# Kernel optimization log

Hardware: AMD Instinct MI355X
Metric: run time of the kernel (lower is better)

The kernel has to match this reference:

```python
import jax, jax.numpy as jnp
import numpy as np

NZ = 1024       # opts.nz (== NH so layer-0 input weights stack with other layers)
NH = 1024       # opts.nh
NSTATE = 64     # opts.n_state
NLAYERS = 4
MAX_PRIM_LEN = 100
T = MAX_PRIM_LEN + 1   # max_unroll=True runs exactly max_prim_len+1 steps
P_BIAS = 1.0           # opts.dec_p_bias


def setup_inputs() -> dict:
    key = jax.random.key(0)
    ks = jax.random.split(key, 9)
    s_ih = 1.0 / np.sqrt(NH)
    u = lambda k, shape: jax.random.uniform(k, shape, jnp.float32, -s_ih, s_ih)
    return {
        "z": jax.random.normal(ks[0], (1, NZ), jnp.float32),
        # torch LSTM params, gate order (i, f, g, o); layer0 input dim == NZ == NH
        "Wih": u(ks[1], (NLAYERS, 4 * NH, NH)),
        "Whh": u(ks[2], (NLAYERS, 4 * NH, NH)),
        "bih": u(ks[3], (NLAYERS, 4 * NH)),
        "bhh": u(ks[4], (NLAYERS, 4 * NH)),
        "Ws": u(ks[5], (NSTATE, NH)),
        "bs": u(ks[6], (NSTATE,)),
        "Wp": u(ks[7], (2, NH)),
        "bp": u(ks[8], (2,)),
    }


def reference(z, Wih, Whh, bih, bhh, Ws, bs, Wp, bp):
    z0 = z.reshape(-1)  # (NZ,)
    zeros = jnp.zeros_like(z0)

    def step(carry, i):
        h, c = carry                      # each (NLAYERS, NH)
        x = jnp.where(i == 0, z0, zeros)  # input is z at t=0, zeros after
        hs, cs = [], []
        inp = x
        for l in range(NLAYERS):
            gates = Wih[l] @ inp + bih[l] + Whh[l] @ h[l] + bhh[l]
            gi, gf, gg, go = jnp.split(gates, 4)
            cl = jax.nn.sigmoid(gf) * c[l] + jax.nn.sigmoid(gi) * jnp.tanh(gg)
            hl = jax.nn.sigmoid(go) * jnp.tanh(cl)
            hs.append(hl)
            cs.append(cl)
            inp = hl
        o = inp                            # top-layer output, (NH,)
        s = Ws @ o + bs                    # state head, (NSTATE,)
        logits = (Wp @ o + bp).at[0].add(P_BIAS)
        p = jax.nn.softmax(logits)         # (2,)
        last = i == T - 1                  # torch: t > max_prim_len -> force [0,1]
        p = jnp.where(last, jnp.array([0.0, 1.0], p.dtype), p)
        samp = jnp.where(last, 1, 0).astype(jnp.int64)  # max_unroll forces 0 until last
        return (jnp.stack(hs), jnp.stack(cs)), (s, p, samp)

    h0 = jnp.zeros((NLAYERS, NH), z.dtype)
    _, (states, probs, samples) = jax.lax.scan(step, (h0, h0), jnp.arange(T))
    return states[:, None, :], probs[:, None, :], samples[:, None]
```

## Files before the change

### kernel.cpp

```cpp
#include <hip/hip_runtime.h>


#define TT    101
#define NBLK  256
#define NTH   512
#define NREP  8
#define SLAB_U32 512
#define HB16_BYTES (4 * TT * NREP * SLAB_U32 * 4)
#define OUT_PROBS 6464
#define OUT_SAMP  6666
#define SENT 0xFFFFFFFFu

typedef _Float16 h2 __attribute__((ext_vector_type(2)));

__device__ __forceinline__ h2 mkh2(float a, float b) {
    h2 r; r.x = (_Float16)a; r.y = (_Float16)b; return r;
}
__device__ __forceinline__ unsigned pack2(float a, float b) {
    return __builtin_bit_cast(unsigned, mkh2(a, b));
}
__device__ __forceinline__ h2 as_h2(unsigned u) { return __builtin_bit_cast(h2, u); }

#if __has_builtin(__builtin_amdgcn_fdot2)
__device__ __forceinline__ float fdot2(h2 a, h2 b, float c) {
    return __builtin_amdgcn_fdot2(a, b, c, false);
}
#else
__device__ __forceinline__ float fdot2(h2 a, h2 b, float c) {
    return fmaf((float)a.x, (float)b.x, fmaf((float)a.y, (float)b.y, c));
}
#endif

__device__ __forceinline__ uint4 load16_bypass(const uint4* p) {
    uint4 r;
    asm volatile("global_load_dwordx4 %0, %1, off sc0 sc1\n\ts_waitcnt vmcnt(0)"
                 : "=v"(r) : "v"(p) : "memory");
    return r;
}
__device__ __forceinline__ void store4_bypass(unsigned* p, unsigned v) {
    asm volatile("global_store_dword %0, %1, off sc0 sc1" :: "v"(p), "v"(v) : "memory");
}
__device__ __forceinline__ uint4 poll16(const uint4* p) {
    uint4 r = load16_bypass(p);
    while (r.x == SENT || r.y == SENT || r.z == SENT || r.w == SENT) {
        __builtin_amdgcn_s_sleep(1);
        r = load16_bypass(p);
    }
    return r;
}

__device__ __forceinline__ float wave_sum(float x) {
    int v;
    v = __builtin_amdgcn_update_dpp(0, __builtin_bit_cast(int, x), 0x111, 0xf, 0xf, false);
    x += __builtin_bit_cast(float, v);
    v = __builtin_amdgcn_update_dpp(0, __builtin_bit_cast(int, x), 0x112, 0xf, 0xf, false);
    x += __builtin_bit_cast(float, v);
    v = __builtin_amdgcn_update_dpp(0, __builtin_bit_cast(int, x), 0x114, 0xf, 0xe, false);
    x += __builtin_bit_cast(float, v);
    v = __builtin_amdgcn_update_dpp(0, __builtin_bit_cast(int, x), 0x118, 0xf, 0xc, false);
    x += __builtin_bit_cast(float, v);
    v = __builtin_amdgcn_update_dpp(0, __builtin_bit_cast(int, x), 0x142, 0xa, 0xf, false);
    x += __builtin_bit_cast(float, v);
    v = __builtin_amdgcn_update_dpp(0, __builtin_bit_cast(int, x), 0x143, 0xc, 0xf, false);
    x += __builtin_bit_cast(float, v);
    return __builtin_bit_cast(float, __builtin_amdgcn_readlane(__builtin_bit_cast(int, x), 63));
}

__device__ __forceinline__ float sigm(float x) { return 1.f / (1.f + expf(-x)); }

__global__ __launch_bounds__(NTH, 2) void lstm_kernel(
    const float* __restrict__ z,
    const float* __restrict__ Wih, const float* __restrict__ Whh,
    const float* __restrict__ bih, const float* __restrict__ bhh,
    const float* __restrict__ Ws,  const float* __restrict__ bs,
    const float* __restrict__ Wp,  const float* __restrict__ bp,
    unsigned* __restrict__ hb16, float* __restrict__ out)
{
    const int tid  = threadIdx.x;
    const int wv   = tid >> 6;
    const int lane = tid & 63;
    const int l    = blockIdx.x >> 6;
    const int gb   = blockIdx.x & 63;
    const int uA   = (gb << 4) + (wv << 1);

    __shared__ __align__(16) uint4 vh4[256];
    __shared__ unsigned hout[8];

    h2 w[8][16];
    #pragma unroll
    for (int r = 0; r < 8; ++r) {
        const int u = uA + (r >> 2);
        const int g = r & 3;
        const size_t row = ((size_t)((l << 12) + (g << 10) + u)) << 10;
        const float4* pa = (const float4*)(Whh + row + (lane << 3));
        const float4* pb = (const float4*)(Whh + row + 512 + (lane << 3));
        const float4* pc = (const float4*)(Wih + row + (lane << 3));
        const float4* pd = (const float4*)(Wih + row + 512 + (lane << 3));
        float4 f;
        f = pa[0]; w[r][0]  = mkh2(f.x, f.y); w[r][1]  = mkh2(f.z, f.w);
        f = pa[1]; w[r][2]  = mkh2(f.x, f.y); w[r][3]  = mkh2(f.z, f.w);
        f = pb[0]; w[r][4]  = mkh2(f.x, f.y); w[r][5]  = mkh2(f.z, f.w);
        f = pb[1]; w[r][6]  = mkh2(f.x, f.y); w[r][7]  = mkh2(f.z, f.w);
        f = pc[0]; w[r][8]  = mkh2(f.x, f.y); w[r][9]  = mkh2(f.z, f.w);
        f = pc[1]; w[r][10] = mkh2(f.x, f.y); w[r][11] = mkh2(f.z, f.w);
        f = pd[0]; w[r][12] = mkh2(f.x, f.y); w[r][13] = mkh2(f.z, f.w);
        f = pd[1]; w[r][14] = mkh2(f.x, f.y); w[r][15] = mkh2(f.z, f.w);
    }

    float bA[4], bB[4];
    #pragma unroll
    for (int g = 0; g < 4; ++g) {
        const int iA = (l << 12) + (g << 10) + uA;
        bA[g] = bih[iA] + bhh[iA];
        bB[g] = bih[iA + 1] + bhh[iA + 1];
    }

    const bool role_states = (l == 0 && wv == 6);
    const bool role_probs  = (l == 1 && gb == 0 && wv == 6);
    float hw0[16], hw1[16], hb0 = 0.f, hb1 = 0.f;
    if (role_states) {
        #pragma unroll
        for (int k = 0; k < 16; ++k) hw0[k] = Ws[(gb << 10) + (lane << 4) + k];
        hb0 = bs[gb];
    } else if (role_probs) {
        #pragma unroll
        for (int k = 0; k < 16; ++k) {
            hw0[k] = Wp[(lane << 4) + k];
            hw1[k] = Wp[1024 + (lane << 4) + k];
        }
        hb0 = bp[0]; hb1 = bp[1];
    }
    int th = 0;

    float cstA = 0.f, cstB = 0.f;

    #pragma unroll 1
    for (int t = 0; t < TT; ++t) {
        const bool full = (l > 0) || (t == 0);
        const int rep = (gb + wv) & (NREP - 1);

        if (wv < 2) {
            const int c = (wv << 6) + lane;
            if (t == 0) vh4[c] = make_uint4(0, 0, 0, 0);
            else {
                const uint4* slab = (const uint4*)(hb16 + (size_t)((l * TT + t - 1) * NREP + rep) * SLAB_U32);
                vh4[c] = poll16(slab + c);
            }
        } else if (wv < 4) {
            const int c = ((wv - 2) << 6) + lane;
            if (l > 0) {
                const uint4* slab = (const uint4*)(hb16 + (size_t)(((l - 1) * TT + t) * NREP + rep) * SLAB_U32);
                vh4[128 + c] = poll16(slab + c);
            } else if (t == 0) {
                const float4 f0 = *(const float4*)(z + (c << 3));
                const float4 f1 = *(const float4*)(z + (c << 3) + 4);
                vh4[128 + c] = make_uint4(pack2(f0.x, f0.y), pack2(f0.z, f0.w),
                                          pack2(f1.x, f1.y), pack2(f1.z, f1.w));
            }
        }
        __syncthreads();

        float acc[8] = {0.f, 0.f, 0.f, 0.f, 0.f, 0.f, 0.f, 0.f};
        {
            const uint4 A1 = vh4[lane];
            const uint4 A2 = vh4[64 + lane];
            const unsigned a8[8] = {A1.x, A1.y, A1.z, A1.w, A2.x, A2.y, A2.z, A2.w};
            #pragma unroll
            for (int k = 0; k < 8; ++k) {
                const h2 v2 = as_h2(a8[k]);
                #pragma unroll
                for (int r = 0; r < 8; ++r) acc[r] = fdot2(w[r][k], v2, acc[r]);
            }
            if (full) {
                const uint4 B1 = vh4[128 + lane];
                const uint4 B2 = vh4[192 + lane];
                const unsigned b8[8] = {B1.x, B1.y, B1.z, B1.w, B2.x, B2.y, B2.z, B2.w};
                #pragma unroll
                for (int k = 0; k < 8; ++k) {
                    const h2 v2 = as_h2(b8[k]);
                    #pragma unroll
                    for (int r = 0; r < 8; ++r) acc[r] = fdot2(w[r][8 + k], v2, acc[r]);
                }
            }
        }

        float tot[8];
        #pragma unroll
        for (int r = 0; r < 8; ++r) tot[r] = wave_sum(acc[r]);

        cstA = fmaf(sigm(tot[1] + bA[1]), cstA, sigm(tot[0] + bA[0]) * tanhf(tot[2] + bA[2]));
        cstB = fmaf(sigm(tot[5] + bB[1]), cstB, sigm(tot[4] + bB[0]) * tanhf(tot[6] + bB[2]));
        const float hA = sigm(tot[3] + bA[3]) * tanhf(cstA);
        const float hB = sigm(tot[7] + bB[3]) * tanhf(cstB);
        if (lane == 0) hout[wv] = pack2(hA, hB);
        __syncthreads();

        if (wv == 7) {
            const unsigned val = hout[lane & 7];
            unsigned* addr = hb16 + (size_t)(l * TT + t) * NREP * SLAB_U32
                           + (size_t)(lane >> 3) * SLAB_U32 + (gb << 3) + (lane & 7);
            store4_bypass(addr, val);
        } else if ((role_states || role_probs) && th < TT && th <= t - 3) {
            const int hrep = (gb + th) & (NREP - 1);
            const uint4* slab3 = (const uint4*)(hb16 + (size_t)((3 * TT + th) * NREP + hrep) * SLAB_U32);
            const uint4 r0 = load16_bypass(slab3 + (lane << 1));
            const uint4 r1 = load16_bypass(slab3 + (lane << 1) + 1);
            const bool ok = !(r0.x == SENT || r0.y == SENT || r0.z == SENT || r0.w == SENT ||
                              r1.x == SENT || r1.y == SENT || r1.z == SENT || r1.w == SENT);
            if (__ballot(ok) == ~0ull) {
                const unsigned u8[8] = {r0.x, r0.y, r0.z, r0.w, r1.x, r1.y, r1.z, r1.w};
                if (role_states) {
                    float a = 0.f;
                    #pragma unroll
                    for (int j = 0; j < 8; ++j) {
                        const h2 p = as_h2(u8[j]);
                        a = fmaf(hw0[2 * j], (float)p.x, a);
                        a = fmaf(hw0[2 * j + 1], (float)p.y, a);
                    }
                    const float tots = wave_sum(a);
                    if (lane == 0) out[th * 64 + gb] = tots + hb0;
                } else {
                    float a0 = 0.f, a1 = 0.f;
                    #pragma unroll
                    for (int j = 0; j < 8; ++j) {
                        const h2 p = as_h2(u8[j]);
                        a0 = fmaf(hw0[2 * j], (float)p.x, a0); a0 = fmaf(hw0[2 * j + 1], (float)p.y, a0);
                        a1 = fmaf(hw1[2 * j], (float)p.x, a1); a1 = fmaf(hw1[2 * j + 1], (float)p.y, a1);
                    }
                    const float t0 = wave_sum(a0), t1 = wave_sum(a1);
                    if (lane == 0) {
                        float p0, p1;
                        if (th == TT - 1) { p0 = 0.f; p1 = 1.f; }
                        else {
                            const float l0 = t0 + hb0 + 1.0f;
                            const float l1 = t1 + hb1;
                            const float m  = fmaxf(l0, l1);
                            const float e0 = expf(l0 - m), e1 = expf(l1 - m);
                            const float inv = 1.f / (e0 + e1);
                            p0 = e0 * inv; p1 = e1 * inv;
                        }
                        out[OUT_PROBS + 2 * th]     = p0;
                        out[OUT_PROBS + 2 * th + 1] = p1;
                        out[OUT_SAMP + th] = (th == TT - 1) ? 1.0f : 0.0f;
                    }
                }
                ++th;
            }
        }
    }

    if (role_states || role_probs) {
        while (th < TT) {
            const int hrep = (gb + th) & (NREP - 1);
            const uint4* slab3 = (const uint4*)(hb16 + (size_t)((3 * TT + th) * NREP + hrep) * SLAB_U32);
            const uint4 r0 = poll16(slab3 + (lane << 1));
            const uint4 r1 = poll16(slab3 + (lane << 1) + 1);
            const unsigned u8[8] = {r0.x, r0.y, r0.z, r0.w, r1.x, r1.y, r1.z, r1.w};
            if (role_states) {
                float a = 0.f;
                #pragma unroll
                for (int j = 0; j < 8; ++j) {
                    const h2 p = as_h2(u8[j]);
                    a = fmaf(hw0[2 * j], (float)p.x, a);
                    a = fmaf(hw0[2 * j + 1], (float)p.y, a);
                }
                const float tots = wave_sum(a);
                if (lane == 0) out[th * 64 + gb] = tots + hb0;
            } else {
                float a0 = 0.f, a1 = 0.f;
                #pragma unroll
                for (int j = 0; j < 8; ++j) {
                    const h2 p = as_h2(u8[j]);
                    a0 = fmaf(hw0[2 * j], (float)p.x, a0); a0 = fmaf(hw0[2 * j + 1], (float)p.y, a0);
                    a1 = fmaf(hw1[2 * j], (float)p.x, a1); a1 = fmaf(hw1[2 * j + 1], (float)p.y, a1);
                }
                const float t0 = wave_sum(a0), t1 = wave_sum(a1);
                if (lane == 0) {
                    float p0, p1;
                    if (th == TT - 1) { p0 = 0.f; p1 = 1.f; }
                    else {
                        const float l0 = t0 + hb0 + 1.0f;
                        const float l1 = t1 + hb1;
                        const float m  = fmaxf(l0, l1);
                        const float e0 = expf(l0 - m), e1 = expf(l1 - m);
                        const float inv = 1.f / (e0 + e1);
                        p0 = e0 * inv; p1 = e1 * inv;
                    }
                    out[OUT_PROBS + 2 * th]     = p0;
                    out[OUT_PROBS + 2 * th + 1] = p1;
                    out[OUT_SAMP + th] = (th == TT - 1) ? 1.0f : 0.0f;
                }
            }
            ++th;
        }
    }
}

extern "C" void kernel_launch(void* const* d_in, const int* in_sizes, int n_in,
                              void* d_out, int out_size, void* d_ws, size_t ws_size,
                              hipStream_t stream)
{
    const float* z   = (const float*)d_in[0];
    const float* Wih = (const float*)d_in[1];
    const float* Whh = (const float*)d_in[2];
    const float* bih = (const float*)d_in[3];
    const float* bhh = (const float*)d_in[4];
    const float* Ws  = (const float*)d_in[5];
    const float* bs  = (const float*)d_in[6];
    const float* Wp  = (const float*)d_in[7];
    const float* bp  = (const float*)d_in[8];
    float* out = (float*)d_out;

    unsigned* hb16 = (unsigned*)d_ws;

    hipMemsetAsync(hb16, 0xFF, HB16_BYTES, stream);
    lstm_kernel<<<NBLK, NTH, 0, stream>>>(z, Wih, Whh, bih, bhh,
                                          Ws, bs, Wp, bp, hb16, out);
}
```

Baseline: 512.4 us.

## Move output heads to dedicated blocks, double-buffer LDS, use fast gate math

```diff
diff --git a/kernel.cpp b/kernel.cpp
--- a/kernel.cpp
+++ b/kernel.cpp
@@ -3,10 +3,12 @@
 
 #define TT    101
 #define NBLK  256
+#define NHEAD 65
 #define NTH   512
 #define NREP  8
 #define SLAB_U32 512
-#define HB16_BYTES (4 * TT * NREP * SLAB_U32 * 4)
+#define STEP_U32 (NREP * SLAB_U32)
+#define HB16_BYTES (4 * TT * STEP_U32 * 4)
 #define OUT_PROBS 6464
 #define OUT_SAMP  6666
 #define SENT 0xFFFFFFFFu
@@ -29,6 +31,18 @@
 __device__ __forceinline__ float fdot2(h2 a, h2 b, float c) {
     return fmaf((float)a.x, (float)b.x, fmaf((float)a.y, (float)b.y, c));
 }
+#endif
+
+#if __has_builtin(__builtin_amdgcn_exp2f) && __has_builtin(__builtin_amdgcn_rcpf)
+__device__ __forceinline__ float fsigm(float x) {
+    return __builtin_amdgcn_rcpf(1.f + __builtin_amdgcn_exp2f(-1.442695041f * x));
+}
+__device__ __forceinline__ float ftanh(float x) {
+    return fmaf(-2.f, __builtin_amdgcn_rcpf(1.f + __builtin_amdgcn_exp2f(2.885390082f * x)), 1.f);
+}
+#else
+__device__ __forceinline__ float fsigm(float x) { return 1.f / (1.f + expf(-x)); }
+__device__ __forceinline__ float ftanh(float x) { return tanhf(x); }
 #endif
 
 __device__ __forceinline__ uint4 load16_bypass(const uint4* p) {
@@ -65,8 +79,6 @@
     x += __builtin_bit_cast(float, v);
     return __builtin_bit_cast(float, __builtin_amdgcn_readlane(__builtin_bit_cast(int, x), 63));
 }
-
-__device__ __forceinline__ float sigm(float x) { return 1.f / (1.f + expf(-x)); }
 
 __global__ __launch_bounds__(NTH, 2) void lstm_kernel(
     const float* __restrict__ z,
@@ -79,12 +91,73 @@
     const int tid  = threadIdx.x;
     const int wv   = tid >> 6;
     const int lane = tid & 63;
-    const int l    = blockIdx.x >> 6;
-    const int gb   = blockIdx.x & 63;
-    const int uA   = (gb << 4) + (wv << 1);
-
-    __shared__ __align__(16) uint4 vh4[256];
-    __shared__ unsigned hout[8];
+
+    if (blockIdx.x >= NBLK) {
+        if (wv != 0) return;
+        const int hb  = blockIdx.x - NBLK;
+        const int rep = hb & (NREP - 1);
+        if (hb < 64) {
+            float wr[16];
+            #pragma unroll
+            for (int k = 0; k < 16; ++k) wr[k] = Ws[(hb << 10) + (lane << 4) + k];
+            const float bsv = bs[hb];
+            for (int th = 0; th < TT; ++th) {
+                const uint4* slab = (const uint4*)(hb16 + (size_t)(3 * TT + th) * STEP_U32 + rep * SLAB_U32);
+                const uint4 r0 = poll16(slab + 2 * lane);
+                const uint4 r1 = poll16(slab + 2 * lane + 1);
+                const unsigned u8[8] = {r0.x, r0.y, r0.z, r0.w, r1.x, r1.y, r1.z, r1.w};
+                float a = 0.f;
+                #pragma unroll
+                for (int j = 0; j < 8; ++j) {
+                    const h2 p = as_h2(u8[j]);
+                    a = fmaf(wr[2 * j], (float)p.x, a);
+                    a = fmaf(wr[2 * j + 1], (float)p.y, a);
+                }
+                a = wave_sum(a);
+                if (lane == 0) out[th * 64 + hb] = a + bsv;
+            }
+        } else {
+            for (int i = lane; i < TT; i += 64) out[OUT_SAMP + i] = (i == TT - 1) ? 1.0f : 0.0f;
+            if (lane == 0) { out[OUT_PROBS + 2 * (TT - 1)] = 0.f; out[OUT_PROBS + 2 * (TT - 1) + 1] = 1.f; }
+            float w0[16], w1[16];
+            #pragma unroll
+            for (int k = 0; k < 16; ++k) {
+                w0[k] = Wp[(lane << 4) + k];
+                w1[k] = Wp[1024 + (lane << 4) + k];
+            }
+            const float bp0 = bp[0], bp1 = bp[1];
+            for (int th = 0; th < TT - 1; ++th) {
+                const uint4* slab = (const uint4*)(hb16 + (size_t)(3 * TT + th) * STEP_U32 + rep * SLAB_U32);
+                const uint4 r0 = poll16(slab + 2 * lane);
+                const uint4 r1 = poll16(slab + 2 * lane + 1);
+                const unsigned u8[8] = {r0.x, r0.y, r0.z, r0.w, r1.x, r1.y, r1.z, r1.w};
+                float a0 = 0.f, a1 = 0.f;
+                #pragma unroll
+                for (int j = 0; j < 8; ++j) {
+                    const h2 p = as_h2(u8[j]);
+                    a0 = fmaf(w0[2 * j], (float)p.x, a0); a0 = fmaf(w0[2 * j + 1], (float)p.y, a0);
+                    a1 = fmaf(w1[2 * j], (float)p.x, a1); a1 = fmaf(w1[2 * j + 1], (float)p.y, a1);
+                }
+                a0 = wave_sum(a0); a1 = wave_sum(a1);
+                if (lane == 0) {
+                    const float l0 = a0 + bp0 + 1.0f;
+                    const float l1 = a1 + bp1;
+                    const float m  = fmaxf(l0, l1);
+                    const float e0 = expf(l0 - m), e1 = expf(l1 - m);
+                    const float inv = 1.f / (e0 + e1);
+                    out[OUT_PROBS + 2 * th]     = e0 * inv;
+                    out[OUT_PROBS + 2 * th + 1] = e1 * inv;
+                }
+            }
+        }
+        return;
+    }
+
+    const int l   = blockIdx.x >> 6;
+    const int gb  = blockIdx.x & 63;
+    const int uA  = (gb << 4) + (wv << 1);
+
+    __shared__ __align__(16) uint4 vbuf[2][256];
 
     h2 w[8][16];
     #pragma unroll
@@ -115,43 +188,28 @@
         bB[g] = bih[iA + 1] + bhh[iA + 1];
     }
 
-    const bool role_states = (l == 0 && wv == 6);
-    const bool role_probs  = (l == 1 && gb == 0 && wv == 6);
-    float hw0[16], hw1[16], hb0 = 0.f, hb1 = 0.f;
-    if (role_states) {
-        #pragma unroll
-        for (int k = 0; k < 16; ++k) hw0[k] = Ws[(gb << 10) + (lane << 4) + k];
-        hb0 = bs[gb];
-    } else if (role_probs) {
-        #pragma unroll
-        for (int k = 0; k < 16; ++k) {
-            hw0[k] = Wp[(lane << 4) + k];
-            hw1[k] = Wp[1024 + (lane << 4) + k];
-        }
-        hb0 = bp[0]; hb1 = bp[1];
-    }
-    int th = 0;
-
     float cstA = 0.f, cstB = 0.f;
 
     #pragma unroll 1
     for (int t = 0; t < TT; ++t) {
         const bool full = (l > 0) || (t == 0);
-        const int rep = (gb + wv) & (NREP - 1);
+        uint4* vh4 = vbuf[t & 1];
 
         if (wv < 2) {
             const int c = (wv << 6) + lane;
             if (t == 0) vh4[c] = make_uint4(0, 0, 0, 0);
             else {
-                const uint4* slab = (const uint4*)(hb16 + (size_t)((l * TT + t - 1) * NREP + rep) * SLAB_U32);
+                const int rep = (gb + wv) & (NREP - 1);
+                const uint4* slab = (const uint4*)(hb16 + (size_t)(l * TT + t - 1) * STEP_U32 + rep * SLAB_U32);
                 vh4[c] = poll16(slab + c);
             }
-        } else if (wv < 4) {
+        } else if (wv < 4 && full) {
             const int c = ((wv - 2) << 6) + lane;
             if (l > 0) {
-                const uint4* slab = (const uint4*)(hb16 + (size_t)(((l - 1) * TT + t) * NREP + rep) * SLAB_U32);
+                const int rep = (gb + wv) & (NREP - 1);
+                const uint4* slab = (const uint4*)(hb16 + (size_t)((l - 1) * TT + t) * STEP_U32 + rep * SLAB_U32);
                 vh4[128 + c] = poll16(slab + c);
-            } else if (t == 0) {
+            } else {
                 const float4 f0 = *(const float4*)(z + (c << 3));
                 const float4 f1 = *(const float4*)(z + (c << 3) + 4);
                 vh4[128 + c] = make_uint4(pack2(f0.x, f0.y), pack2(f0.z, f0.w),
@@ -188,110 +246,16 @@
         #pragma unroll
         for (int r = 0; r < 8; ++r) tot[r] = wave_sum(acc[r]);
 
-        cstA = fmaf(sigm(tot[1] + bA[1]), cstA, sigm(tot[0] + bA[0]) * tanhf(tot[2] + bA[2]));
-        cstB = fmaf(sigm(tot[5] + bB[1]), cstB, sigm(tot[4] + bB[0]) * tanhf(tot[6] + bB[2]));
-        const float hA = sigm(tot[3] + bA[3]) * tanhf(cstA);
-        const float hB = sigm(tot[7] + bB[3]) * tanhf(cstB);
-        if (lane == 0) hout[wv] = pack2(hA, hB);
-        __syncthreads();
-
-        if (wv == 7) {
-            const unsigned val = hout[lane & 7];
-            unsigned* addr = hb16 + (size_t)(l * TT + t) * NREP * SLAB_U32
-                           + (size_t)(lane >> 3) * SLAB_U32 + (gb << 3) + (lane & 7);
-            store4_bypass(addr, val);
-        } else if ((role_states || role_probs) && th < TT && th <= t - 3) {
-            const int hrep = (gb + th) & (NREP - 1);
-            const uint4* slab3 = (const uint4*)(hb16 + (size_t)((3 * TT + th) * NREP + hrep) * SLAB_U32);
-            const uint4 r0 = load16_bypass(slab3 + (lane << 1));
-            const uint4 r1 = load16_bypass(slab3 + (lane << 1) + 1);
-            const bool ok = !(r0.x == SENT || r0.y == SENT || r0.z == SENT || r0.w == SENT ||
-                              r1.x == SENT || r1.y == SENT || r1.z == SENT || r1.w == SENT);
-            if (__ballot(ok) == ~0ull) {
-                const unsigned u8[8] = {r0.x, r0.y, r0.z, r0.w, r1.x, r1.y, r1.z, r1.w};
-                if (role_states) {
-                    float a = 0.f;
-                    #pragma unroll
-                    for (int j = 0; j < 8; ++j) {
-                        const h2 p = as_h2(u8[j]);
-                        a = fmaf(hw0[2 * j], (float)p.x, a);
-                        a = fmaf(hw0[2 * j + 1], (float)p.y, a);
-                    }
-                    const float tots = wave_sum(a);
-                    if (lane == 0) out[th * 64 + gb] = tots + hb0;
-                } else {
-                    float a0 = 0.f, a1 = 0.f;
-                    #pragma unroll
-                    for (int j = 0; j < 8; ++j) {
-                        const h2 p = as_h2(u8[j]);
-                        a0 = fmaf(hw0[2 * j], (float)p.x, a0); a0 = fmaf(hw0[2 * j + 1], (float)p.y, a0);
-                        a1 = fmaf(hw1[2 * j], (float)p.x, a1); a1 = fmaf(hw1[2 * j + 1], (float)p.y, a1);
-                    }
-                    const float t0 = wave_sum(a0), t1 = wave_sum(a1);
-                    if (lane == 0) {
-                        float p0, p1;
-                        if (th == TT - 1) { p0 = 0.f; p1 = 1.f; }
-                        else {
-                            const float l0 = t0 + hb0 + 1.0f;
-                            const float l1 = t1 + hb1;
-                            const float m  = fmaxf(l0, l1);
-                            const float e0 = expf(l0 - m), e1 = expf(l1 - m);
-                            const float inv = 1.f / (e0 + e1);
-                            p0 = e0 * inv; p1 = e1 * inv;
-                        }
-                        out[OUT_PROBS + 2 * th]     = p0;
-                        out[OUT_PROBS + 2 * th + 1] = p1;
-                        out[OUT_SAMP + th] = (th == TT - 1) ? 1.0f : 0.0f;
-                    }
-                }
-                ++th;
-            }
-        }
-    }
-
-    if (role_states || role_probs) {
-        while (th < TT) {
-            const int hrep = (gb + th) & (NREP - 1);
-            const uint4* slab3 = (const uint4*)(hb16 + (size_t)((3 * TT + th) * NREP + hrep) * SLAB_U32);
-            const uint4 r0 = poll16(slab3 + (lane << 1));
-            const uint4 r1 = poll16(slab3 + (lane << 1) + 1);
-            const unsigned u8[8] = {r0.x, r0.y, r0.z, r0.w, r1.x, r1.y, r1.z, r1.w};
-            if (role_states) {
-                float a = 0.f;
-                #pragma unroll
-                for (int j = 0; j < 8; ++j) {
-                    const h2 p = as_h2(u8[j]);
-                    a = fmaf(hw0[2 * j], (float)p.x, a);
-                    a = fmaf(hw0[2 * j + 1], (float)p.y, a);
-                }
-                const float tots = wave_sum(a);
-                if (lane == 0) out[th * 64 + gb] = tots + hb0;
-            } else {
-                float a0 = 0.f, a1 = 0.f;
-                #pragma unroll
-                for (int j = 0; j < 8; ++j) {
-                    const h2 p = as_h2(u8[j]);
-                    a0 = fmaf(hw0[2 * j], (float)p.x, a0); a0 = fmaf(hw0[2 * j + 1], (float)p.y, a0);
-                    a1 = fmaf(hw1[2 * j], (float)p.x, a1); a1 = fmaf(hw1[2 * j + 1], (float)p.y, a1);
-                }
-                const float t0 = wave_sum(a0), t1 = wave_sum(a1);
-                if (lane == 0) {
-                    float p0, p1;
-                    if (th == TT - 1) { p0 = 0.f; p1 = 1.f; }
-                    else {
-                        const float l0 = t0 + hb0 + 1.0f;
-                        const float l1 = t1 + hb1;
-                        const float m  = fmaxf(l0, l1);
-                        const float e0 = expf(l0 - m), e1 = expf(l1 - m);
-                        const float inv = 1.f / (e0 + e1);
-                        p0 = e0 * inv; p1 = e1 * inv;
-                    }
-                    out[OUT_PROBS + 2 * th]     = p0;
-                    out[OUT_PROBS + 2 * th + 1] = p1;
-                    out[OUT_SAMP + th] = (th == TT - 1) ? 1.0f : 0.0f;
-                }
-            }
-            ++th;
+        cstA = fmaf(fsigm(tot[1] + bA[1]), cstA, fsigm(tot[0] + bA[0]) * ftanh(tot[2] + bA[2]));
+        cstB = fmaf(fsigm(tot[5] + bB[1]), cstB, fsigm(tot[4] + bB[0]) * ftanh(tot[6] + bB[2]));
+        const float hA = fsigm(tot[3] + bA[3]) * ftanh(cstA);
+        const float hB = fsigm(tot[7] + bB[3]) * ftanh(cstB);
+
+        const unsigned packed = pack2(hA, hB);
+        if (lane < NREP) {
+            unsigned* addr = hb16 + (size_t)(l * TT + t) * STEP_U32
+                           + (lane << 9) + (gb << 3) + wv;
+            store4_bypass(addr, packed);
         }
     }
 }
@@ -314,6 +278,6 @@
     unsigned* hb16 = (unsigned*)d_ws;
 
     hipMemsetAsync(hb16, 0xFF, HB16_BYTES, stream);
-    lstm_kernel<<<NBLK, NTH, 0, stream>>>(z, Wih, Whh, bih, bhh,
-                                          Ws, bs, Wp, bp, hb16, out);
-}
+    lstm_kernel<<<NBLK + NHEAD, NTH, 0, stream>>>(z, Wih, Whh, bih, bhh,
+                                                  Ws, bs, Wp, bp, hb16, out);
+}
```

Result: slower. 543.8 us (+6.1%).
